# Optimization experiments

Hardware: AMD Instinct MI355X
Metric: run time of the kernel (lower is better)

Reference implementation:

```python
import jax, jax.numpy as jnp
import numpy as np

B, T, DEMO = 64, 4096, 8
N_MOD, N_POS = 37, 10
D_IN = N_POS + 1 + N_MOD  # 48
PHI_W, LATENT = 128, 128
PSI_W, PSI_L = 128, 128
DOT, HEADS = 64, 4
RHO_W, OUT = 128, 1
MAX_TIME = 1000.0


def _dense_init(key, fan_in, fan_out):
    lim = float(np.sqrt(6.0 / fan_in))  # he_uniform-ish
    return jax.random.uniform(key, (fan_in, fan_out), jnp.float32, -lim, lim)


def setup_inputs() -> dict:
    key = jax.random.key(0)
    ks = jax.random.split(key, 32)
    inp = {}
    inp['demo'] = jax.random.normal(ks[0], (B, DEMO), jnp.float32)
    inp['times'] = jax.random.uniform(ks[1], (B, T, 1), jnp.float32, 0.0, 100.0)
    inp['values'] = jax.random.normal(ks[2], (B, T, 1), jnp.float32)
    inp['measurements'] = jax.random.randint(ks[3], (B, T), 0, N_MOD, jnp.int32)
    # all sequences full length -> N = B*(T+1) static
    inp['segment_ids'] = jnp.repeat(jnp.arange(B, dtype=jnp.int32), T + 1)
    inp['timescales'] = jnp.asarray(MAX_TIME ** np.linspace(0.0, 1.0, N_POS // 2), jnp.float32)
    inp['demo_W1'] = _dense_init(ks[4], DEMO, PHI_W); inp['demo_b1'] = jnp.zeros((PHI_W,), jnp.float32)
    inp['demo_W2'] = _dense_init(ks[5], PHI_W, D_IN); inp['demo_b2'] = jnp.zeros((D_IN,), jnp.float32)
    dims = [D_IN, PHI_W, PHI_W, PHI_W, LATENT]
    for i in range(4):
        inp['phi_W%d' % i] = _dense_init(ks[6 + i], dims[i], dims[i + 1])
        inp['phi_b%d' % i] = jnp.zeros((dims[i + 1],), jnp.float32)
    pdims = [D_IN, PSI_W, PSI_W, PSI_L]
    for i in range(3):
        inp['psi_W%d' % i] = _dense_init(ks[10 + i], pdims[i], pdims[i + 1])
        inp['psi_b%d' % i] = jnp.zeros((pdims[i + 1],), jnp.float32)
    inp['W_k'] = _dense_init(ks[13], PSI_L + D_IN, DOT * HEADS)
    # original inits W_q to zeros (degenerate uniform attention); small random keeps test non-trivial
    inp['W_q'] = jax.random.normal(ks[14], (HEADS, DOT), jnp.float32) * 0.05
    rdims = [LATENT * HEADS, RHO_W, RHO_W, RHO_W, OUT]
    for i in range(4):
        inp['rho_W%d' % i] = _dense_init(ks[15 + i], rdims[i], rdims[i + 1])
        inp['rho_b%d' % i] = jnp.zeros((rdims[i + 1],), jnp.float32)
    return inp


def _forward(demo, times, values, timescales,
             demo_W1, demo_b1, demo_W2, demo_b2,
             phi_W0, phi_b0, phi_W1, phi_b1, phi_W2, phi_b2, phi_W3, phi_b3,
             psi_W0, psi_b0, psi_W1, psi_b1, psi_W2, psi_b2,
             W_k, W_q,
             rho_W0, rho_b0, rho_W1, rho_b1, rho_W2, rho_b2, rho_W3, rho_b3,
             measurements, segment_ids):
    relu = jax.nn.relu
    nseg = demo.shape[0]
    # positional encoding: times [B,T,1] / timescales [5] -> sin|cos -> [B,T,10]
    scaled = times / timescales[None, None, :]
    tt = jnp.concatenate([jnp.sin(scaled), jnp.cos(scaled)], axis=-1)
    meas = jax.nn.one_hot(measurements, N_MOD, dtype=times.dtype)  # [B,T,37]
    combined = jnp.concatenate([tt, values, meas], axis=-1)        # [B,T,48]
    demo_enc = relu(demo @ demo_W1 + demo_b1) @ demo_W2 + demo_b2  # [B,48]
    x = jnp.concatenate([demo_enc[:, None, :], combined], axis=1)  # [B,T+1,48]
    collected = x.reshape(-1, x.shape[-1])                         # [N,48]
    # phi MLP -> encoded [N,LATENT]
    h = collected
    for W, b in ((phi_W0, phi_b0), (phi_W1, phi_b1), (phi_W2, phi_b2), (phi_W3, phi_b3)):
        h = relu(h @ W + b)
    encoded = h
    # psi MLP -> [N,PSI_L], then per-segment mean, scattered back
    p = collected
    for W, b in ((psi_W0, psi_b0), (psi_W1, psi_b1), (psi_W2, psi_b2)):
        p = relu(p @ W + b)
    seg_sum = jax.ops.segment_sum(p, segment_ids, num_segments=nseg)
    counts = jax.ops.segment_sum(jnp.ones((p.shape[0],), p.dtype), segment_ids, num_segments=nseg)
    agg = seg_sum / counts[:, None]
    comb2 = jnp.concatenate([collected, agg[segment_ids]], axis=-1)  # [N, 48+128]
    keys = (comb2 @ W_k).reshape(-1, HEADS, DOT)                     # [N,H,D]
    preattn = jnp.einsum('nhd,hd->nh', keys, W_q) / jnp.sqrt(jnp.float32(DOT))
    # segment softmax per head
    m = jax.ops.segment_max(preattn, segment_ids, num_segments=nseg)
    e = jnp.exp(preattn - m[segment_ids])
    s = jax.ops.segment_sum(e, segment_ids, num_segments=nseg)
    attn = e / s[segment_ids]                                        # [N,H]
    # head-major weighted concat: [N, H*LATENT]
    weighted = (attn[:, :, None] * encoded[:, None, :]).reshape(-1, HEADS * LATENT)
    agg_out = jax.ops.segment_sum(weighted, segment_ids, num_segments=nseg)  # [B,512]
    r = agg_out
    for W, b in ((rho_W0, rho_b0), (rho_W1, rho_b1), (rho_W2, rho_b2)):
        r = relu(r @ W + b)
    return jax.nn.sigmoid(r @ rho_W3 + rho_b3)  # [B,1]


def reference(demo, times, values, timescales,
              demo_W1, demo_b1, demo_W2, demo_b2,
              phi_W0, phi_b0, phi_W1, phi_b1, phi_W2, phi_b2, phi_W3, phi_b3,
              psi_W0, psi_b0, psi_W1, psi_b1, psi_W2, psi_b2,
              W_k, W_q,
              rho_W0, rho_b0, rho_W1, rho_b1, rho_W2, rho_b2, rho_W3, rho_b3,
              measurements, segment_ids):
    return _forward(demo, times, values, timescales,
                    demo_W1, demo_b1, demo_W2, demo_b2,
                    phi_W0, phi_b0, phi_W1, phi_b1, phi_W2, phi_b2, phi_W3, phi_b3,
                    psi_W0, psi_b0, psi_W1, psi_b1, psi_W2, psi_b2,
                    W_k, W_q,
                    rho_W0, rho_b0, rho_W1, rho_b1, rho_W2, rho_b2, rho_W3, rho_b3,
                    measurements, segment_ids)
```

## Files before the change

kernel.cpp:

```cpp
#include <hip/hip_runtime.h>
#include <hip/hip_bf16.h>
#include <math.h>


#define BSEG 64
#define TLEN 4096
#define NPART 9
#define PART_STRIDE 520

#define OFF_DEMO 0
#define OFF_WQ   3072
#define OFF_WT   3264
#define OFF_PARTIALS 31936

typedef __attribute__((ext_vector_type(8))) short short8;
typedef __attribute__((ext_vector_type(4))) float f32x4;
typedef __attribute__((ext_vector_type(2))) float f32x2;

static __device__ __forceinline__ float bfbits2f(unsigned v) { return __uint_as_float(v << 16); }
static __device__ __forceinline__ unsigned short f2bf_rne(float x) {
  unsigned u = __float_as_uint(x);
  unsigned r = (u + 0x7FFFu + ((u >> 16) & 1u)) >> 16;
  return (unsigned short)r;
}
static __device__ __forceinline__ unsigned pk2(float a, float b) {
  float2 f2 = make_float2(a, b);
  __hip_bfloat162 h = __float22bfloat162_rn(f2);
  unsigned u;
  __builtin_memcpy(&u, &h, 4);
  return u;
}

__global__ __launch_bounds__(256) void k_prep(
    const float* __restrict__ demo, const float* __restrict__ dW1, const float* __restrict__ db1,
    const float* __restrict__ dW2, const float* __restrict__ db2,
    const float* __restrict__ Wk, const float* __restrict__ Wq,
    const float* __restrict__ W0, const float* __restrict__ W1,
    const float* __restrict__ W2, const float* __restrict__ W3,
    float* __restrict__ ws) {
  __shared__ float drow[8];
  __shared__ float hdrow[128];
  int bid = blockIdx.x, tid = threadIdx.x;
  if (bid < 224) {
    unsigned short* wt = (unsigned short*)(ws + OFF_WT);
    int i = bid * 256 + tid;
    float v;
    if (i < 8192) {
      int n = i >> 6, k = i & 63;
      v = (k < 48) ? W0[k * 128 + n] : 0.f;
    } else {
      int j = i - 8192;
      int l = j >> 14, r = j & 16383;
      int n = r >> 7, k = r & 127;
      const float* W = (l == 0) ? W1 : (l == 1) ? W2 : W3;
      v = W[k * 128 + n];
    }
    wt[i] = f2bf_rne(v);
    return;
  }
  if (bid == 224) {
    if (tid < 192) {
      int i = tid >> 2, h = tid & 3;
      float a = 0.f;
      for (int d = 0; d < 64; ++d) a = fmaf(Wk[i * 256 + h * 64 + d], Wq[h * 64 + d], a);
      ws[OFF_WQ + tid] = a * 0.125f;
    }
    return;
  }
  int r = bid - 225;
  if (tid < 8) drow[tid] = demo[r * 8 + tid];
  __syncthreads();
  if (tid < 128) {
    float a = db1[tid];
#pragma unroll
    for (int i = 0; i < 8; ++i) a = fmaf(drow[i], dW1[i * 128 + tid], a);
    hdrow[tid] = fmaxf(a, 0.f);
  }
  __syncthreads();
  if (tid < 48) {
    float a = db2[tid];
    for (int k = 0; k < 128; ++k) a = fmaf(hdrow[k], dW2[k * 48 + tid], a);
    ws[OFF_DEMO + r * 48 + tid] = a;
  }
}

template<int MT>
static __device__ __forceinline__ void mfma_layer_T(
    const unsigned short* hin, unsigned short* hout,
    const short8 (&Wf)[2][4], const f32x4 (&bias4)[2],
    int l16, int quad, int n0) {
  const f32x4 z4 = {0.f, 0.f, 0.f, 0.f};
#pragma unroll
  for (int mt = 0; mt < MT; ++mt) {
    short8 Bv[4];
#pragma unroll
    for (int s = 0; s < 4; ++s)
      Bv[s] = *(const short8*)(hin + (mt * 16 + l16) * 136 + s * 32 + quad * 8);
    f32x4 a0 = bias4[0], a1 = bias4[1];
    __builtin_amdgcn_s_setprio(1);
#pragma unroll
    for (int s = 0; s < 4; ++s) {
      a0 = __builtin_amdgcn_mfma_f32_16x16x32_bf16(Wf[0][s], Bv[s], a0, 0, 0, 0);
      a1 = __builtin_amdgcn_mfma_f32_16x16x32_bf16(Wf[1][s], Bv[s], a1, 0, 0, 0);
    }
    __builtin_amdgcn_s_setprio(0);
    f32x4 r0 = __builtin_elementwise_max(a0, z4);
    f32x4 r1 = __builtin_elementwise_max(a1, z4);
    uint4 o;
    o.x = pk2(r0[0], r0[1]);
    o.y = pk2(r0[2], r0[3]);
    o.z = pk2(r1[0], r1[1]);
    o.w = pk2(r1[2], r1[3]);
    *(uint4*)(hout + (mt * 16 + l16) * 136 + n0 + quad * 8) = o;
  }
}
template<int MT>
static __device__ __forceinline__ void mfma_layer0_T(
    const unsigned short* cin, unsigned short* hout,
    const short8 (&Wf)[2][2], const f32x4 (&bias4)[2],
    int l16, int quad, int n0) {
  const f32x4 z4 = {0.f, 0.f, 0.f, 0.f};
#pragma unroll
  for (int mt = 0; mt < MT; ++mt) {
    short8 Bv[2];
#pragma unroll
    for (int s = 0; s < 2; ++s)
      Bv[s] = *(const short8*)(cin + (mt * 16 + l16) * 72 + s * 32 + quad * 8);
    f32x4 a0 = bias4[0], a1 = bias4[1];
    __builtin_amdgcn_s_setprio(1);
    a0 = __builtin_amdgcn_mfma_f32_16x16x32_bf16(Wf[0][0], Bv[0], a0, 0, 0, 0);
    a0 = __builtin_amdgcn_mfma_f32_16x16x32_bf16(Wf[0][1], Bv[1], a0, 0, 0, 0);
    a1 = __builtin_amdgcn_mfma_f32_16x16x32_bf16(Wf[1][0], Bv[0], a1, 0, 0, 0);
    a1 = __builtin_amdgcn_mfma_f32_16x16x32_bf16(Wf[1][1], Bv[1], a1, 0, 0, 0);
    __builtin_amdgcn_s_setprio(0);
    f32x4 r0 = __builtin_elementwise_max(a0, z4);
    f32x4 r1 = __builtin_elementwise_max(a1, z4);
    uint4 o;
    o.x = pk2(r0[0], r0[1]);
    o.y = pk2(r0[2], r0[3]);
    o.z = pk2(r1[0], r1[1]);
    o.w = pk2(r1[2], r1[3]);
    *(uint4*)(hout + (mt * 16 + l16) * 136 + n0 + quad * 8) = o;
  }
}

__global__ __launch_bounds__(256, 2) void k_main(
    const float* __restrict__ times, const float* __restrict__ values,
    const int* __restrict__ meas, const float* __restrict__ tsc,
    const float* __restrict__ ws,
    const float* __restrict__ b0g, const float* __restrict__ b1g,
    const float* __restrict__ b2g, const float* __restrict__ b3g,
    float* __restrict__ part) {
  __shared__ __align__(16) unsigned short hA[128 * 136];
  __shared__ __align__(16) unsigned short hB[128 * 136];
  __shared__ __align__(16) float preb[512 * 4];
  __shared__ __align__(16) float wql[192];
  __shared__ float mred[16];
  int tid = threadIdx.x;
  const int lane = tid & 63, wv = tid >> 6, quad = lane >> 4, l16 = lane & 15;
  const int n0 = wv * 32;

  const unsigned short* wt = (const unsigned short*)(ws + OFF_WT);
  short8 B0[2][2], B1[2][4], B2[2][4], B3[2][4];
  f32x4 bias0[2], bias1[2], bias2[2];
  float bias3[2];
#pragma unroll
  for (int t = 0; t < 2; ++t) {
    int n  = n0 + ((l16 >> 2) << 3) + t * 4 + (l16 & 3);
    int nq = n0 + quad * 8 + t * 4;
    bias0[t] = *(const f32x4*)(b0g + nq);
    bias1[t] = *(const f32x4*)(b1g + nq);
    bias2[t] = *(const f32x4*)(b2g + nq);
    bias3[t] = b3g[n];
#pragma unroll
    for (int s = 0; s < 2; ++s)
      B0[t][s] = *(const short8*)(wt + n * 64 + s * 32 + quad * 8);
#pragma unroll
    for (int s = 0; s < 4; ++s) {
      B1[t][s] = *(const short8*)(wt + 8192  + n * 128 + s * 32 + quad * 8);
      B2[t][s] = *(const short8*)(wt + 24576 + n * 128 + s * 32 + quad * 8);
      B3[t][s] = *(const short8*)(wt + 40960 + n * 128 + s * 32 + quad * 8);
    }
  }
  if (tid < 192) wql[tid] = ws[OFF_WQ + tid];
  __syncthreads();

  if (blockIdx.x == 512) {
    {
      int r = tid >> 2, cs = tid & 3;
      unsigned short seg[16];
#pragma unroll
      for (int i = 0; i < 16; ++i) seg[i] = 0;
      if (cs < 3)
#pragma unroll
        for (int i = 0; i < 16; ++i) seg[i] = f2bf_rne(ws[OFF_DEMO + r * 48 + cs * 16 + i]);
      unsigned u[8];
#pragma unroll
      for (int i = 0; i < 8; ++i) u[i] = (unsigned)seg[2 * i] | ((unsigned)seg[2 * i + 1] << 16);
      uint4* dst = (uint4*)(hB + r * 72 + cs * 16);
      dst[0] = make_uint4(u[0], u[1], u[2], u[3]);
      dst[1] = make_uint4(u[4], u[5], u[6], u[7]);
    }
    {
      int r = tid >> 2, h = tid & 3;
      float a = 0.f;
      for (int i = 0; i < 48; ++i) a = fmaf(ws[OFF_DEMO + r * 48 + i], wql[i * 4 + h], a);
      preb[tid] = __expf(a);
    }
    f32x4 bias34[2];
#pragma unroll
    for (int t = 0; t < 2; ++t) bias34[t] = *(const f32x4*)(b3g + n0 + quad * 8 + t * 4);
    __syncthreads();
    mfma_layer0_T<4>(hB, hA, B0, bias0, l16, quad, n0); __syncthreads();
    mfma_layer_T<4>(hA, hB, B1, bias1, l16, quad, n0); __syncthreads();
    mfma_layer_T<4>(hB, hA, B2, bias2, l16, quad, n0); __syncthreads();
    mfma_layer_T<4>(hA, hB, B3, bias34, l16, quad, n0); __syncthreads();
    {
      int r = tid >> 2, h = tid & 3;
      part[(r * NPART + 8) * PART_STRIDE + 4 + h] = preb[tid];
    }
    for (int i = tid; i < 64 * 512; i += 256) {
      int r = i >> 9, rem = i & 511;
      int h = rem >> 7, l = rem & 127;
      part[(r * NPART + 8) * PART_STRIDE + 8 + rem] =
          preb[r * 4 + h] * bfbits2f(hB[r * 136 + l]);
    }
    return;
  }

  int b = blockIdx.x >> 3, c = blockIdx.x & 7;
  int t0 = c << 9;
  float invts[5];
#pragma unroll
  for (int i = 0; i < 5; ++i) invts[i] = 1.f / tsc[i];

  float s4[4] = {0.f, 0.f, 0.f, 0.f};
  unsigned usv0[8], usv1[8];
  const f32x4* wql4 = (const f32x4*)wql;
#pragma unroll
  for (int rr = 0; rr < 2; ++rr) {
    int r = tid + rr * 256;
    int t = t0 + r;
    float tv = times[b * TLEN + t];
    float vvv = values[b * TLEN + t];
    int mm = meas[b * TLEN + t];
    float f[11];
#pragma unroll
    for (int i = 0; i < 5; ++i) { float s = tv * invts[i]; f[i] = __sinf(s); f[5 + i] = __cosf(s); }
    f[10] = vvv;
    f32x4 a4 = wql4[11 + mm];
#pragma unroll
    for (int i = 0; i < 11; ++i) {
      f32x4 fi = {f[i], f[i], f[i], f[i]};
      a4 = __builtin_elementwise_fma(fi, wql4[i], a4);
    }
    float e0 = __expf(a4[0]), e1 = __expf(a4[1]);
    float e2 = __expf(a4[2]), e3 = __expf(a4[3]);
    *(f32x4*)(preb + r * 4) = (f32x4){e0, e1, e2, e3};
    s4[0] += e0; s4[1] += e1; s4[2] += e2; s4[3] += e3;
    int kk = 11 + mm;
    unsigned uu[8];
    uu[0] = pk2(f[0], f[1]); uu[1] = pk2(f[2], f[3]);
    uu[2] = pk2(f[4], f[5]); uu[3] = pk2(f[6], f[7]);
    uu[4] = pk2(f[8], f[9]);
    uu[5] = pk2(f[10], (kk == 11) ? 1.f : 0.f);
    uu[6] = ((kk == 12) ? 0x3F80u : 0u) | ((kk == 13) ? 0x3F800000u : 0u);
    uu[7] = ((kk == 14) ? 0x3F80u : 0u) | ((kk == 15) ? 0x3F800000u : 0u);
    if (rr == 0) {
#pragma unroll
      for (int k = 0; k < 8; ++k) usv0[k] = uu[k];
    } else {
#pragma unroll
      for (int k = 0; k < 8; ++k) usv1[k] = uu[k];
    }
  }

  auto build_tile = [&](int tile) {
    int r = tid & 127;
    if (((tid >> 7) & 1) == (tile & 1)) {
      unsigned uw[8];
#pragma unroll
      for (int k = 0; k < 8; ++k) uw[k] = (tile & 2) ? usv1[k] : usv0[k];
      uint4* dst = (uint4*)(hB + r * 72);
      dst[0] = make_uint4(uw[0], uw[1], uw[2], uw[3]);
      dst[1] = make_uint4(uw[4], uw[5], uw[6], uw[7]);
      uint4 z = make_uint4(0u, 0u, 0u, 0u);
      *(uint4*)(hB + r * 72 + 48) = z;
      *(uint4*)(hB + r * 72 + 56) = z;
    } else {
      int t = t0 + tile * 128 + r;
      int mm = meas[b * TLEN + t];
      int kk = 11 + mm;
      uint4 z = make_uint4(0u, 0u, 0u, 0u);
      uint4* dst = (uint4*)(hB + r * 72 + 16);
#pragma unroll
      for (int k = 0; k < 4; ++k) dst[k] = z;
      asm volatile("" ::: "memory");
      if (kk >= 16) hB[r * 72 + kk] = 0x3F80;
    }
  };

  f32x2 pacc2[2][2] = {{{0.f, 0.f}, {0.f, 0.f}}, {{0.f, 0.f}, {0.f, 0.f}}};
  const f32x4 z4 = {0.f, 0.f, 0.f, 0.f};
  const int ncb = n0 + ((l16 >> 2) << 3) + (l16 & 3);
  build_tile(0);
  for (int tile = 0; tile < 4; ++tile) {
    int rb = tile << 7;
    __syncthreads();
    mfma_layer0_T<8>(hB, hA, B0, bias0, l16, quad, n0); __syncthreads();
    mfma_layer_T<8>(hA, hB, B1, bias1, l16, quad, n0); __syncthreads();
    mfma_layer_T<8>(hB, hA, B2, bias2, l16, quad, n0); __syncthreads();
    if (tile < 3) build_tile(tile + 1);
#pragma unroll
    for (int mt = 0; mt < 8; ++mt) {
      short8 A[4];
#pragma unroll
      for (int s = 0; s < 4; ++s)
        A[s] = *(const short8*)(hA + (mt * 16 + l16) * 136 + s * 32 + quad * 8);
      f32x4 acc0 = {bias3[0], bias3[0], bias3[0], bias3[0]};
      f32x4 acc1 = {bias3[1], bias3[1], bias3[1], bias3[1]};
      __builtin_amdgcn_s_setprio(1);
#pragma unroll
      for (int s = 0; s < 4; ++s) {
        acc0 = __builtin_amdgcn_mfma_f32_16x16x32_bf16(A[s], B3[0][s], acc0, 0, 0, 0);
        acc1 = __builtin_amdgcn_mfma_f32_16x16x32_bf16(A[s], B3[1][s], acc1, 0, 0, 0);
      }
      __builtin_amdgcn_s_setprio(0);
      f32x4 r0 = __builtin_elementwise_max(acc0, z4);
      f32x4 r1 = __builtin_elementwise_max(acc1, z4);
#pragma unroll
      for (int j = 0; j < 4; ++j) {
        int row = rb + mt * 16 + quad * 4 + j;
        f32x4 e4 = *(const f32x4*)(preb + row * 4);
        f32x2 e01 = {e4[0], e4[1]}, e23 = {e4[2], e4[3]};
        f32x2 v0 = {r0[j], r0[j]}, v1 = {r1[j], r1[j]};
        pacc2[0][0] = __builtin_elementwise_fma(v0, e01, pacc2[0][0]);
        pacc2[0][1] = __builtin_elementwise_fma(v0, e23, pacc2[0][1]);
        pacc2[1][0] = __builtin_elementwise_fma(v1, e01, pacc2[1][0]);
        pacc2[1][1] = __builtin_elementwise_fma(v1, e23, pacc2[1][1]);
      }
    }
  }
  float pacc[2][4];
#pragma unroll
  for (int t = 0; t < 2; ++t)
#pragma unroll
    for (int h = 0; h < 4; ++h) pacc[t][h] = pacc2[t][h >> 1][h & 1];
#pragma unroll
  for (int t = 0; t < 2; ++t)
#pragma unroll
    for (int h = 0; h < 4; ++h) {
      float v = pacc[t][h];
      v += __shfl_xor(v, 16, 64);
      v += __shfl_xor(v, 32, 64);
      pacc[t][h] = v;
    }
#pragma unroll
  for (int off = 32; off > 0; off >>= 1)
#pragma unroll
    for (int h = 0; h < 4; ++h) s4[h] += __shfl_xor(s4[h], off, 64);
  if (lane == 0)
#pragma unroll
    for (int h = 0; h < 4; ++h) mred[wv * 4 + h] = s4[h];
  __syncthreads();
  float* P = part + (b * NPART + c) * PART_STRIDE;
  if (tid < 4) P[4 + tid] = mred[tid] + mred[4 + tid] + mred[8 + tid] + mred[12 + tid];
  if (quad == 0)
#pragma unroll
    for (int t = 0; t < 2; ++t)
#pragma unroll
      for (int h = 0; h < 4; ++h)
        P[8 + h * 128 + (ncb + t * 4)] = pacc[t][h];
}

__global__ __launch_bounds__(256) void k_combine(
    const float* __restrict__ part,
    const float* __restrict__ rW0, const float* __restrict__ rb0,
    const float* __restrict__ rW1, const float* __restrict__ rb1,
    const float* __restrict__ rW2, const float* __restrict__ rb2,
    const float* __restrict__ rW3, const float* __restrict__ rb3,
    float* __restrict__ out) {
  __shared__ float Ss[4], agg[512], r1[128], p0[256];
  int tid = threadIdx.x;
  int b = blockIdx.x;
  const float* P = part + b * NPART * PART_STRIDE;
  if (tid < 4) {
    float s = 0.f;
    for (int p = 0; p < NPART; ++p) s += P[p * PART_STRIDE + 4 + tid];
    Ss[tid] = s;
  }
  __syncthreads();
  for (int idx = tid; idx < 512; idx += 256) {
    int h = idx >> 7;
    float a = 0.f;
    for (int p = 0; p < NPART; ++p) a += P[p * PART_STRIDE + 8 + idx];
    agg[idx] = a / Ss[h];
  }
  __syncthreads();
  const int col = tid & 127, half = tid >> 7;
  {
    float a = 0.f;
    for (int k = half * 256; k < half * 256 + 256; ++k) a = fmaf(agg[k], rW0[k * 128 + col], a);
    p0[tid] = a;
  }
  __syncthreads();
  if (tid < 128) r1[tid] = fmaxf(rb0[tid] + p0[tid] + p0[128 + tid], 0.f);
  __syncthreads();
  {
    float a = 0.f;
    for (int k = half * 64; k < half * 64 + 64; ++k) a = fmaf(r1[k], rW1[k * 128 + col], a);
    p0[tid] = a;
  }
  __syncthreads();
  if (tid < 128) r1[tid] = fmaxf(rb1[tid] + p0[tid] + p0[128 + tid], 0.f);
  __syncthreads();
  {
    float a = 0.f;
    for (int k = half * 64; k < half * 64 + 64; ++k) a = fmaf(r1[k], rW2[k * 128 + col], a);
    p0[tid] = a;
  }
  __syncthreads();
  if (tid < 128) p0[tid] = fmaxf(rb2[tid] + p0[tid] + p0[128 + tid], 0.f) * rW3[tid];
  __syncthreads();
  if (tid < 64) {
    float v = p0[tid] + p0[tid + 64];
#pragma unroll
    for (int off = 32; off > 0; off >>= 1) v += __shfl_xor(v, off, 64);
    if (tid == 0) out[b] = 1.f / (1.f + __expf(-(rb3[0] + v)));
  }
}

extern "C" void kernel_launch(void* const* d_in, const int* in_sizes, int n_in,
                              void* d_out, int out_size, void* d_ws, size_t ws_size,
                              hipStream_t stream) {
  const float* demo   = (const float*)d_in[0];
  const float* times  = (const float*)d_in[1];
  const float* values = (const float*)d_in[2];
  const int*   meas   = (const int*)d_in[3];
  const float* tsc = (const float*)d_in[5];
  const float* dW1 = (const float*)d_in[6];
  const float* db1 = (const float*)d_in[7];
  const float* dW2 = (const float*)d_in[8];
  const float* db2 = (const float*)d_in[9];
  const float* pW0 = (const float*)d_in[10];
  const float* pb0 = (const float*)d_in[11];
  const float* pW1 = (const float*)d_in[12];
  const float* pb1 = (const float*)d_in[13];
  const float* pW2 = (const float*)d_in[14];
  const float* pb2 = (const float*)d_in[15];
  const float* pW3 = (const float*)d_in[16];
  const float* pb3 = (const float*)d_in[17];
  const float* Wk  = (const float*)d_in[24];
  const float* Wq  = (const float*)d_in[25];
  const float* rW0 = (const float*)d_in[26];
  const float* rb0 = (const float*)d_in[27];
  const float* rW1 = (const float*)d_in[28];
  const float* rb1 = (const float*)d_in[29];
  const float* rW2 = (const float*)d_in[30];
  const float* rb2 = (const float*)d_in[31];
  const float* rW3 = (const float*)d_in[32];
  const float* rb3 = (const float*)d_in[33];
  float* ws = (float*)d_ws;
  float* partials = ws + OFF_PARTIALS;

  k_prep<<<289, 256, 0, stream>>>(demo, dW1, db1, dW2, db2, Wk, Wq,
                                  pW0, pW1, pW2, pW3, ws);
  k_main<<<513, 256, 0, stream>>>(times, values, meas, tsc, ws,
                                  pb0, pb1, pb2, pb3, partials);
  k_combine<<<64, 256, 0, stream>>>(partials, rW0, rb0, rW1, rb1, rW2, rb2, rW3, rb3,
                                    (float*)d_out);
}
```

Before: 183.3 us.

## Split each sequence into 16 chunks with 64-row tiles for more blocks

Doubles the main kernel grid from 513 to 1025 blocks by giving each block 256 timesteps instead of 512. Each block processes four 64-row tiles, so shared buffers shrink and launch bounds allow four blocks per CU. The goal is more parallelism and better latency hiding across the GPU's CUs. In exchange, the combine kernel has twice as many partials to reduce, and each block's fixed cost of loading the weight fragments is paid twice as often. The input loads are also hoisted ahead of the weight loads so they overlap.

Result: slower. 248.8 us (+35.7%).

```diff
diff --git a/kernel.cpp b/kernel.cpp
--- a/kernel.cpp
+++ b/kernel.cpp
@@ -5,7 +5,7 @@
 
 #define BSEG 64
 #define TLEN 4096
-#define NPART 9
+#define NPART 17
 #define PART_STRIDE 520
 
 #define OFF_DEMO 0
@@ -144,21 +144,35 @@
   }
 }
 
-__global__ __launch_bounds__(256, 2) void k_main(
+__global__ __launch_bounds__(256, 4) void k_main(
     const float* __restrict__ times, const float* __restrict__ values,
     const int* __restrict__ meas, const float* __restrict__ tsc,
     const float* __restrict__ ws,
     const float* __restrict__ b0g, const float* __restrict__ b1g,
     const float* __restrict__ b2g, const float* __restrict__ b3g,
     float* __restrict__ part) {
-  __shared__ __align__(16) unsigned short hA[128 * 136];
-  __shared__ __align__(16) unsigned short hB[128 * 136];
-  __shared__ __align__(16) float preb[512 * 4];
+  __shared__ __align__(16) unsigned short hA[64 * 136];
+  __shared__ __align__(16) unsigned short hB[64 * 136];
+  __shared__ __align__(16) float preb[256 * 4];
   __shared__ __align__(16) float wql[192];
   __shared__ float mred[16];
   int tid = threadIdx.x;
   const int lane = tid & 63, wv = tid >> 6, quad = lane >> 4, l16 = lane & 15;
   const int n0 = wv * 32;
+
+  const int b = blockIdx.x >> 4, c = blockIdx.x & 15;
+  const int t0 = c << 8;
+  float tv = 0.f, vvv = 0.f;
+  int mm = 0;
+  float invts[5];
+  if (blockIdx.x < 1024) {
+    int t = t0 + tid;
+    tv = times[b * TLEN + t];
+    vvv = values[b * TLEN + t];
+    mm = meas[b * TLEN + t];
+#pragma unroll
+    for (int i = 0; i < 5; ++i) invts[i] = 1.f / tsc[i];
+  }
 
   const unsigned short* wt = (const unsigned short*)(ws + OFF_WT);
   short8 B0[2][2], B1[2][4], B2[2][4], B3[2][4];
@@ -185,7 +199,7 @@
   if (tid < 192) wql[tid] = ws[OFF_WQ + tid];
   __syncthreads();
 
-  if (blockIdx.x == 512) {
+  if (blockIdx.x == 1024) {
     {
       int r = tid >> 2, cs = tid & 3;
       unsigned short seg[16];
@@ -217,33 +231,21 @@
     mfma_layer_T<4>(hA, hB, B3, bias34, l16, quad, n0); __syncthreads();
     {
       int r = tid >> 2, h = tid & 3;
-      part[(r * NPART + 8) * PART_STRIDE + 4 + h] = preb[tid];
+      part[(r * NPART + 16) * PART_STRIDE + 4 + h] = preb[tid];
     }
     for (int i = tid; i < 64 * 512; i += 256) {
       int r = i >> 9, rem = i & 511;
       int h = rem >> 7, l = rem & 127;
-      part[(r * NPART + 8) * PART_STRIDE + 8 + rem] =
+      part[(r * NPART + 16) * PART_STRIDE + 8 + rem] =
           preb[r * 4 + h] * bfbits2f(hB[r * 136 + l]);
     }
     return;
   }
 
-  int b = blockIdx.x >> 3, c = blockIdx.x & 7;
-  int t0 = c << 9;
-  float invts[5];
-#pragma unroll
-  for (int i = 0; i < 5; ++i) invts[i] = 1.f / tsc[i];
-
-  float s4[4] = {0.f, 0.f, 0.f, 0.f};
-  unsigned usv0[8], usv1[8];
+  float s4[4];
+  unsigned usv[8];
   const f32x4* wql4 = (const f32x4*)wql;
-#pragma unroll
-  for (int rr = 0; rr < 2; ++rr) {
-    int r = tid + rr * 256;
-    int t = t0 + r;
-    float tv = times[b * TLEN + t];
-    float vvv = values[b * TLEN + t];
-    int mm = meas[b * TLEN + t];
+  {
     float f[11];
 #pragma unroll
     for (int i = 0; i < 5; ++i) { float s = tv * invts[i]; f[i] = __sinf(s); f[5 + i] = __cosf(s); }
@@ -256,41 +258,30 @@
     }
     float e0 = __expf(a4[0]), e1 = __expf(a4[1]);
     float e2 = __expf(a4[2]), e3 = __expf(a4[3]);
-    *(f32x4*)(preb + r * 4) = (f32x4){e0, e1, e2, e3};
-    s4[0] += e0; s4[1] += e1; s4[2] += e2; s4[3] += e3;
+    *(f32x4*)(preb + tid * 4) = (f32x4){e0, e1, e2, e3};
+    s4[0] = e0; s4[1] = e1; s4[2] = e2; s4[3] = e3;
     int kk = 11 + mm;
-    unsigned uu[8];
-    uu[0] = pk2(f[0], f[1]); uu[1] = pk2(f[2], f[3]);
-    uu[2] = pk2(f[4], f[5]); uu[3] = pk2(f[6], f[7]);
-    uu[4] = pk2(f[8], f[9]);
-    uu[5] = pk2(f[10], (kk == 11) ? 1.f : 0.f);
-    uu[6] = ((kk == 12) ? 0x3F80u : 0u) | ((kk == 13) ? 0x3F800000u : 0u);
-    uu[7] = ((kk == 14) ? 0x3F80u : 0u) | ((kk == 15) ? 0x3F800000u : 0u);
-    if (rr == 0) {
-#pragma unroll
-      for (int k = 0; k < 8; ++k) usv0[k] = uu[k];
-    } else {
-#pragma unroll
-      for (int k = 0; k < 8; ++k) usv1[k] = uu[k];
-    }
+    usv[0] = pk2(f[0], f[1]); usv[1] = pk2(f[2], f[3]);
+    usv[2] = pk2(f[4], f[5]); usv[3] = pk2(f[6], f[7]);
+    usv[4] = pk2(f[8], f[9]);
+    usv[5] = pk2(f[10], (kk == 11) ? 1.f : 0.f);
+    usv[6] = ((kk == 12) ? 0x3F80u : 0u) | ((kk == 13) ? 0x3F800000u : 0u);
+    usv[7] = ((kk == 14) ? 0x3F80u : 0u) | ((kk == 15) ? 0x3F800000u : 0u);
   }
 
   auto build_tile = [&](int tile) {
-    int r = tid & 127;
-    if (((tid >> 7) & 1) == (tile & 1)) {
-      unsigned uw[8];
-#pragma unroll
-      for (int k = 0; k < 8; ++k) uw[k] = (tile & 2) ? usv1[k] : usv0[k];
+    int r = lane;
+    if (wv == tile) {
       uint4* dst = (uint4*)(hB + r * 72);
-      dst[0] = make_uint4(uw[0], uw[1], uw[2], uw[3]);
-      dst[1] = make_uint4(uw[4], uw[5], uw[6], uw[7]);
+      dst[0] = make_uint4(usv[0], usv[1], usv[2], usv[3]);
+      dst[1] = make_uint4(usv[4], usv[5], usv[6], usv[7]);
       uint4 z = make_uint4(0u, 0u, 0u, 0u);
       *(uint4*)(hB + r * 72 + 48) = z;
       *(uint4*)(hB + r * 72 + 56) = z;
-    } else {
-      int t = t0 + tile * 128 + r;
-      int mm = meas[b * TLEN + t];
-      int kk = 11 + mm;
+    } else if (wv == (tile ^ 1)) {
+      int t = t0 + tile * 64 + r;
+      int mmf = meas[b * TLEN + t];
+      int kk = 11 + mmf;
       uint4 z = make_uint4(0u, 0u, 0u, 0u);
       uint4* dst = (uint4*)(hB + r * 72 + 16);
 #pragma unroll
@@ -305,14 +296,14 @@
   const int ncb = n0 + ((l16 >> 2) << 3) + (l16 & 3);
   build_tile(0);
   for (int tile = 0; tile < 4; ++tile) {
-    int rb = tile << 7;
+    int rb = tile << 6;
     __syncthreads();
-    mfma_layer0_T<8>(hB, hA, B0, bias0, l16, quad, n0); __syncthreads();
-    mfma_layer_T<8>(hA, hB, B1, bias1, l16, quad, n0); __syncthreads();
-    mfma_layer_T<8>(hB, hA, B2, bias2, l16, quad, n0); __syncthreads();
+    mfma_layer0_T<4>(hB, hA, B0, bias0, l16, quad, n0); __syncthreads();
+    mfma_layer_T<4>(hA, hB, B1, bias1, l16, quad, n0); __syncthreads();
+    mfma_layer_T<4>(hB, hA, B2, bias2, l16, quad, n0); __syncthreads();
     if (tile < 3) build_tile(tile + 1);
 #pragma unroll
-    for (int mt = 0; mt < 8; ++mt) {
+    for (int mt = 0; mt < 4; ++mt) {
       short8 A[4];
 #pragma unroll
       for (int s = 0; s < 4; ++s)
@@ -465,8 +456,8 @@
 
   k_prep<<<289, 256, 0, stream>>>(demo, dW1, db1, dW2, db2, Wk, Wq,
                                   pW0, pW1, pW2, pW3, ws);
-  k_main<<<513, 256, 0, stream>>>(times, values, meas, tsc, ws,
-                                  pb0, pb1, pb2, pb3, partials);
+  k_main<<<1025, 256, 0, stream>>>(times, values, meas, tsc, ws,
+                                   pb0, pb1, pb2, pb3, partials);
   k_combine<<<64, 256, 0, stream>>>(partials, rW0, rb0, rW1, rb1, rW2, rb2, rW3, rb3,
                                     (float*)d_out);
 }
```
